# Kernel tuning notes

Hardware: AMD Instinct MI355X
Metric: run time of the kernel (lower is better)

Reference implementation:

```python
import jax, jax.numpy as jnp
import numpy as np

B, SQ, SK, D, H, HD = 2, 2048, 2048, 1024, 16, 64


def setup_inputs() -> dict:
    key = jax.random.key(0)
    ks = jax.random.split(key, 10)
    s = 1.0 / np.sqrt(D)  # keep activations well-scaled
    return {
        "x": jax.random.normal(ks[0], (B, SQ, D), jnp.float32),
        "encoder_output": jax.random.normal(ks[1], (B, SK, D), jnp.float32),
        "Wq": jax.random.normal(ks[2], (H, D, HD), jnp.float32) * s,
        "bq": jax.random.normal(ks[3], (H, HD), jnp.float32) * 0.01,
        "Wk": jax.random.normal(ks[4], (H, D, HD), jnp.float32) * s,
        "bk": jax.random.normal(ks[5], (H, HD), jnp.float32) * 0.01,
        "Wv": jax.random.normal(ks[6], (H, D, HD), jnp.float32) * s,
        "bv": jax.random.normal(ks[7], (H, HD), jnp.float32) * 0.01,
        "Wo": jax.random.normal(ks[8], (D, D), jnp.float32) * s,
        "bo": jax.random.normal(ks[9], (D,), jnp.float32) * 0.01,
    }


def reference(x, encoder_output, Wq, bq, Wk, bk, Wv, bv, Wo, bo):
    # Batched per-head projections (equivalent to the per-head nn.Linear loop).
    q = jnp.einsum('bsd,hde->bhse', x, Wq) + bq[None, :, None, :]              # [B,H,SQ,HD]
    k = jnp.einsum('bsd,hde->bhse', encoder_output, Wk) + bk[None, :, None, :]  # [B,H,SK,HD]
    v = jnp.einsum('bsd,hde->bhse', encoder_output, Wv) + bv[None, :, None, :]  # [B,H,SK,HD]
    scale = 1.0 / jnp.sqrt(jnp.asarray(HD, q.dtype))
    scores = jnp.einsum('bhqe,bhke->bhqk', q, k) * scale                        # [B,H,SQ,SK]
    attn = jax.nn.softmax(scores, axis=-1)
    out = jnp.einsum('bhqk,bhke->bhqe', attn, v)                                # [B,H,SQ,HD]
    # concat heads along feature dim (head order matches torch.cat order)
    out = out.transpose(0, 2, 1, 3).reshape(out.shape[0], out.shape[2], -1)     # [B,SQ,D]
    # final linear; dropout is identity in eval mode
    return out @ Wo + bo
```

## Files before the change

### kernel.cpp

```cpp
#include <hip/hip_runtime.h>


typedef unsigned short u16;
typedef __bf16 bf16x8 __attribute__((ext_vector_type(8)));
typedef float f32x4 __attribute__((ext_vector_type(4)));

#define B_ 2
#define SQ_ 2048
#define SK_ 2048
#define D_ 1024
#define H_ 16
#define HD_ 64

__device__ __forceinline__ u16 f2bf(float f) {
  union { float f; unsigned u; } c; c.f = f;
  unsigned u = c.u;
  return (u16)((u + 0x7fffu + ((u >> 16) & 1u)) >> 16);
}
__device__ __forceinline__ float bf2f(u16 h) {
  union { unsigned u; float f; } c; c.u = ((unsigned)h) << 16;
  return c.f;
}
__device__ __forceinline__ unsigned pack_bf16(float lo, float hi) {
  union { __bf16 h[2]; unsigned u; } c;
  c.h[0] = (__bf16)lo;
  c.h[1] = (__bf16)hi;
  return c.u;
}

#define GLOAD_LDS16(gp, lp)                                                  \
  __builtin_amdgcn_global_load_lds(                                          \
      (const __attribute__((address_space(1))) void*)(gp),                   \
      (__attribute__((address_space(3))) void*)(lp), 16, 0, 0)

__global__ __launch_bounds__(256) void cast2_f32_bf16(const float* __restrict__ x,
                                                      const float* __restrict__ enc,
                                                      u16* __restrict__ xb,
                                                      u16* __restrict__ eb) {
  const float* in = blockIdx.z ? enc : x;
  u16* out = blockIdx.z ? eb : xb;
  int i = blockIdx.x * 256 + threadIdx.x;
  float4 v = ((const float4*)in)[i];
  uint2 p;
  p.x = (unsigned)f2bf(v.x) | ((unsigned)f2bf(v.y) << 16);
  p.y = (unsigned)f2bf(v.z) | ((unsigned)f2bf(v.w) << 16);
  ((uint2*)out)[i] = p;
}

__global__ __launch_bounds__(256) void wqkv_trans(const float* __restrict__ Wq,
                                                  const float* __restrict__ Wk,
                                                  const float* __restrict__ Wv,
                                                  u16* __restrict__ out) {
  __shared__ float tile[64][65];
  const int mat = blockIdx.z >> 4, head = blockIdx.z & 15;
  const float* W = (mat == 0) ? Wq : (mat == 1 ? Wk : Wv);
  const float* ib = W + (long)head * 65536;
  u16* ob = out + ((long)mat << 20) + (long)head * 65536;
  int r0 = blockIdx.y << 6;
  int tid = threadIdx.x;
#pragma unroll
  for (int i = 0; i < 16; ++i) {
    int idx = tid + (i << 8);
    int r = idx >> 6, c = idx & 63;
    tile[r][c] = ib[(long)(r0 + r) * 64 + c];
  }
  __syncthreads();
#pragma unroll
  for (int i = 0; i < 16; ++i) {
    int idx = tid + (i << 8);
    int cc = idx >> 6, rr = idx & 63;
    ob[(long)cc * 1024 + (r0 + rr)] = f2bf(tile[rr][cc]);
  }
}

__global__ __launch_bounds__(256) void transpose_to_bf16(const float* __restrict__ in,
                                                         u16* __restrict__ out,
                                                         int R, int C,
                                                         long ibs, long obs) {
  __shared__ float tile[64][65];
  const float* ib = in + (long)blockIdx.z * ibs;
  u16* ob = out + (long)blockIdx.z * obs;
  int r0 = blockIdx.y << 6, c0 = blockIdx.x << 6;
  int tid = threadIdx.x;
#pragma unroll
  for (int i = 0; i < 16; ++i) {
    int idx = tid + (i << 8);
    int r = idx >> 6, c = idx & 63;
    tile[r][c] = ib[(long)(r0 + r) * C + (c0 + c)];
  }
  __syncthreads();
#pragma unroll
  for (int i = 0; i < 16; ++i) {
    int idx = tid + (i << 8);
    int cc = idx >> 6, rr = idx & 63;
    ob[(long)(c0 + cc) * R + (r0 + rr)] = f2bf(tile[rr][cc]);
  }
}

__global__ __launch_bounds__(256) void gemm_qkv(const u16* __restrict__ xb,
                                                const u16* __restrict__ eb,
                                                const u16* __restrict__ Wt3,
                                                const float* __restrict__ bq,
                                                const float* __restrict__ bk,
                                                const float* __restrict__ bv,
                                                u16* __restrict__ qws,
                                                u16* __restrict__ kws,
                                                u16* __restrict__ vT) {
  constexpr int M = 2048, N = 1024, K = 1024;
  __shared__ __align__(16) u16 As[128 * 32];
  __shared__ __align__(16) u16 Bs[128 * 32];
  const int tid = threadIdx.x;
  const int lane = tid & 63;
  const int wid = tid >> 6;
  const int l16 = lane & 15, quad = lane >> 4;
  const int wm = wid >> 1, wn = wid & 1;
  const int bn0g = blockIdx.x << 7;
  const int seg = bn0g >> 10;
  const int bn0 = bn0g & (N - 1);
  const int bm0 = blockIdx.y << 7;
  const u16* A = (seg == 0) ? xb : eb;
  const u16* Wt = Wt3 + ((long)seg << 20);
  const float* bias = (seg == 0) ? bq : (seg == 1 ? bk : bv);
  const long abase = (long)blockIdx.z * M * K;

  f32x4 acc[4][4];
#pragma unroll
  for (int i = 0; i < 4; ++i)
#pragma unroll
    for (int j = 0; j < 4; ++j) acc[i][j] = f32x4{0.f, 0.f, 0.f, 0.f};

  const int r0 = tid >> 2;
  const int c0s = (tid & 3) << 3;
  const u16* agp = A + abase + (long)(bm0 + r0) * K + c0s;
  const u16* bgp = Wt + (long)(bn0 + r0) * K + c0s;
  u16* alp = As + tid * 8;
  u16* blp = Bs + tid * 8;

  for (int k0 = 0; k0 < K; k0 += 32) {
    GLOAD_LDS16(agp + k0, alp);
    GLOAD_LDS16(agp + k0 + (long)64 * K, alp + 2048);
    GLOAD_LDS16(bgp + k0, blp);
    GLOAD_LDS16(bgp + k0 + (long)64 * K, blp + 2048);
    __syncthreads();
    bf16x8 af[4], bfr[4];
#pragma unroll
    for (int mi = 0; mi < 4; ++mi)
      af[mi] = *(const bf16x8*)(As + (wm * 64 + mi * 16 + l16) * 32 + quad * 8);
#pragma unroll
    for (int ni = 0; ni < 4; ++ni)
      bfr[ni] = *(const bf16x8*)(Bs + (wn * 64 + ni * 16 + l16) * 32 + quad * 8);
#pragma unroll
    for (int mi = 0; mi < 4; ++mi)
#pragma unroll
      for (int ni = 0; ni < 4; ++ni)
        acc[mi][ni] = __builtin_amdgcn_mfma_f32_16x16x32_bf16(af[mi], bfr[ni],
                                                              acc[mi][ni], 0, 0, 0);
    __syncthreads();
  }

  float bv4[4];
#pragma unroll
  for (int ni = 0; ni < 4; ++ni) bv4[ni] = bias[bn0 + wn * 64 + ni * 16 + l16];

  if (seg == 2) {
    const long zb = (long)blockIdx.z * N * M;
#pragma unroll
    for (int mi = 0; mi < 4; ++mi)
#pragma unroll
      for (int ni = 0; ni < 4; ++ni) {
        int colg = bn0 + wn * 64 + ni * 16 + l16;
        int rowg = bm0 + wm * 64 + mi * 16 + (quad << 2);
        ushort4 pk = make_ushort4(f2bf(acc[mi][ni][0] + bv4[ni]),
                                  f2bf(acc[mi][ni][1] + bv4[ni]),
                                  f2bf(acc[mi][ni][2] + bv4[ni]),
                                  f2bf(acc[mi][ni][3] + bv4[ni]));
        *(ushort4*)(vT + zb + (long)colg * M + rowg) = pk;
      }
  } else {
    u16* outp = seg ? kws : qws;
    const long cbase = (long)blockIdx.z * M * N;
#pragma unroll
    for (int mi = 0; mi < 4; ++mi)
#pragma unroll
      for (int ni = 0; ni < 4; ++ni)
#pragma unroll
        for (int r = 0; r < 4; ++r) {
          int row = bm0 + wm * 64 + mi * 16 + (quad << 2) + r;
          int col = bn0 + wn * 64 + ni * 16 + l16;
          outp[cbase + (long)row * N + col] = f2bf(acc[mi][ni][r] + bv4[ni]);
        }
  }
}

__global__ __launch_bounds__(256) void gemm_final(const u16* __restrict__ A,
                                                  const u16* __restrict__ Wt,
                                                  const float* __restrict__ bias,
                                                  float* __restrict__ C) {
  constexpr int M = 2048, N = 1024, K = 1024;
  __shared__ __align__(16) u16 As[64 * 32];
  __shared__ __align__(16) u16 Bs[128 * 32];
  const int tid = threadIdx.x;
  const int lane = tid & 63;
  const int wid = tid >> 6;
  const int l16 = lane & 15, quad = lane >> 4;
  const int bn0 = blockIdx.x << 7, bm0 = blockIdx.y << 6;

  f32x4 acc[4][2];
#pragma unroll
  for (int i = 0; i < 4; ++i)
#pragma unroll
    for (int j = 0; j < 2; ++j) acc[i][j] = f32x4{0.f, 0.f, 0.f, 0.f};

  const int r0 = tid >> 2;
  const int c0s = (tid & 3) << 3;
  const long abase = (long)blockIdx.z * M * K;
  const u16* agp = A + abase + (long)(bm0 + r0) * K + c0s;
  const u16* bgp = Wt + (long)(bn0 + r0) * K + c0s;
  u16* alp = As + tid * 8;
  u16* blp = Bs + tid * 8;

  for (int k0 = 0; k0 < K; k0 += 32) {
    GLOAD_LDS16(agp + k0, alp);
    GLOAD_LDS16(bgp + k0, blp);
    GLOAD_LDS16(bgp + k0 + (long)64 * K, blp + 2048);
    __syncthreads();
    bf16x8 af[4], bfr[2];
#pragma unroll
    for (int mi = 0; mi < 4; ++mi)
      af[mi] = *(const bf16x8*)(As + (mi * 16 + l16) * 32 + quad * 8);
#pragma unroll
    for (int ni = 0; ni < 2; ++ni)
      bfr[ni] = *(const bf16x8*)(Bs + (wid * 32 + ni * 16 + l16) * 32 + quad * 8);
#pragma unroll
    for (int mi = 0; mi < 4; ++mi)
#pragma unroll
      for (int ni = 0; ni < 2; ++ni)
        acc[mi][ni] = __builtin_amdgcn_mfma_f32_16x16x32_bf16(af[mi], bfr[ni],
                                                              acc[mi][ni], 0, 0, 0);
    __syncthreads();
  }

  float bv2[2];
#pragma unroll
  for (int ni = 0; ni < 2; ++ni) bv2[ni] = bias[bn0 + wid * 32 + ni * 16 + l16];
  const long cbase = (long)blockIdx.z * M * N;
#pragma unroll
  for (int mi = 0; mi < 4; ++mi)
#pragma unroll
    for (int ni = 0; ni < 2; ++ni)
#pragma unroll
      for (int r = 0; r < 4; ++r) {
        int row = bm0 + mi * 16 + (quad << 2) + r;
        int col = bn0 + wid * 32 + ni * 16 + l16;
        C[cbase + (long)row * N + col] = acc[mi][ni][r] + bv2[ni];
      }
}

#define ATTN_STAGE(kpp, vpp, bb)                                             \
  do {                                                                       \
    GLOAD_LDS16((kpp), Ks[bb] + tid * 8);                                    \
    GLOAD_LDS16((kpp) + (long)32 * D_, Ks[bb] + 2048 + tid * 8);             \
    GLOAD_LDS16((vpp), Vs[bb] + tid * 8);                                    \
    GLOAD_LDS16((vpp) + (long)32 * SK_, Vs[bb] + 2048 + tid * 8);            \
  } while (0)

__global__ __launch_bounds__(256, 4) void attn_flash(const u16* __restrict__ q,
                                                     const u16* __restrict__ k,
                                                     const u16* __restrict__ vT,
                                                     u16* __restrict__ ctx) {
  __shared__ __align__(16) u16 Ks[2][64 * 64];
  __shared__ __align__(16) u16 Vs[2][64 * 64];

  const int tid = threadIdx.x;
  const int lane = tid & 63;
  const int wid = tid >> 6;
  const int l16 = lane & 15, quad = lane >> 4;
  const int q0 = (blockIdx.x << 6) + (wid << 4);
  const int h = blockIdx.y, b = blockIdx.z;

  const u16* qp = q + ((long)(b * SQ_ + q0 + l16) * D_ + h * HD_ + quad * 8);
  bf16x8 a0 = *(const bf16x8*)(qp);
  bf16x8 a1 = *(const bf16x8*)(qp + 32);

  const int srow = tid >> 3, sch = tid & 7;
  const int ssw = ((sch ^ (srow & 7)) << 3);
  const u16* kp = k + ((long)(b * SK_ + srow) * D_ + h * HD_ + ssw);
  const u16* vp = vT + ((long)(b * D_ + h * HD_ + srow) * SK_ + ssw);

  const int ksw0 = ((quad ^ (l16 & 7)) << 3);
  const int ksw1 = (((quad + 4) ^ (l16 & 7)) << 3);
  const int srcA = l16 + ((quad & 1) << 5);
  const bool hisel = quad >= 2;

  float ps = 0.f;
  f32x4 o[4];
#pragma unroll
  for (int et = 0; et < 4; ++et) o[et] = f32x4{0.f, 0.f, 0.f, 0.f};

  ATTN_STAGE(kp, vp, 0);
  kp += (long)64 * D_;
  vp += 64;

  for (int c = 0; c < 32; ++c) {
    const int cur = c & 1;
    __syncthreads();
    if (c < 31) {
      ATTN_STAGE(kp, vp, cur ^ 1);
      kp += (long)64 * D_;
      vp += 64;
    }
    const u16* Kb = Ks[cur];
    const u16* Vb = Vs[cur];

    unsigned pk[4][2];
#pragma unroll
    for (int nt = 0; nt < 4; ++nt) {
      const u16* kr = Kb + (((nt << 4) + l16) << 6);
      bf16x8 kf0 = *(const bf16x8*)(kr + ksw0);
      bf16x8 kf1 = *(const bf16x8*)(kr + ksw1);
      f32x4 acc = {0.f, 0.f, 0.f, 0.f};
      acc = __builtin_amdgcn_mfma_f32_16x16x32_bf16(kf0, a0, acc, 0, 0, 0);
      acc = __builtin_amdgcn_mfma_f32_16x16x32_bf16(kf1, a1, acc, 0, 0, 0);
      float p0 = __expf(acc[0] * 0.125f);
      float p1 = __expf(acc[1] * 0.125f);
      float p2 = __expf(acc[2] * 0.125f);
      float p3 = __expf(acc[3] * 0.125f);
      ps += (p0 + p1) + (p2 + p3);
      pk[nt][0] = pack_bf16(p0, p1);
      pk[nt][1] = pack_bf16(p2, p3);
    }

#pragma unroll
    for (int kt = 0; kt < 2; ++kt) {
      int uA0 = __shfl((int)pk[2 * kt][0], srcA, 64);
      int uA1 = __shfl((int)pk[2 * kt + 1][0], srcA, 64);
      int vA0 = __shfl((int)pk[2 * kt][1], srcA, 64);
      int vA1 = __shfl((int)pk[2 * kt + 1][1], srcA, 64);
      int uB0 = __shfl((int)pk[2 * kt][0], srcA + 16, 64);
      int uB1 = __shfl((int)pk[2 * kt + 1][0], srcA + 16, 64);
      int vB0 = __shfl((int)pk[2 * kt][1], srcA + 16, 64);
      int vB1 = __shfl((int)pk[2 * kt + 1][1], srcA + 16, 64);
      union { int u[4]; bf16x8 v; } pa;
      pa.u[0] = hisel ? uA1 : uA0;
      pa.u[1] = hisel ? vA1 : vA0;
      pa.u[2] = hisel ? uB1 : uB0;
      pa.u[3] = hisel ? vB1 : vB0;
#pragma unroll
      for (int et = 0; et < 4; ++et) {
        const int e = (et << 4) + l16;
        bf16x8 bvf = *(const bf16x8*)(Vb + (e << 6) +
                                      ((((kt << 2) + quad) ^ (l16 & 7)) << 3));
        o[et] = __builtin_amdgcn_mfma_f32_16x16x32_bf16(pa.v, bvf, o[et], 0, 0, 0);
      }
    }
  }

  ps += __shfl_xor(ps, 16, 64);
  ps += __shfl_xor(ps, 32, 64);
  float inv = 1.f / ps;
  float dq[4];
#pragma unroll
  for (int r = 0; r < 4; ++r) dq[r] = __shfl(inv, (quad << 2) + r, 64);

#pragma unroll
  for (int et = 0; et < 4; ++et)
#pragma unroll
    for (int r = 0; r < 4; ++r) {
      int row = (quad << 2) + r;
      ctx[(long)(b * SQ_ + q0 + row) * D_ + h * HD_ + et * 16 + l16] =
          f2bf(o[et][r] * dq[r]);
    }
}

extern "C" void kernel_launch(void* const* d_in, const int* in_sizes, int n_in,
                              void* d_out, int out_size, void* d_ws, size_t ws_size,
                              hipStream_t stream) {
  const float* x   = (const float*)d_in[0];
  const float* enc = (const float*)d_in[1];
  const float* Wq  = (const float*)d_in[2];
  const float* bq  = (const float*)d_in[3];
  const float* Wk  = (const float*)d_in[4];
  const float* bk  = (const float*)d_in[5];
  const float* Wv  = (const float*)d_in[6];
  const float* bv  = (const float*)d_in[7];
  const float* Wo  = (const float*)d_in[8];
  const float* bo  = (const float*)d_in[9];

  const long NE_X = (long)B_ * SQ_ * D_;
  const long NE_W = (long)D_ * D_;

  u16* outA = (u16*)d_out;
  u16* outB = outA + NE_X;
  u16* eb  = outB;
  u16* vTp = outA;

  u16* ws  = (u16*)d_ws;
  u16* WqT = ws;
  u16* WoT = WqT + 3 * NE_W;
  u16* qws = WoT + NE_W;
  u16* kws = qws + NE_X;
  u16* xb  = kws + NE_X;
  u16* ctx = xb;

  cast2_f32_bf16<<<dim3((unsigned)(NE_X / 4 / 256), 1, 2), 256, 0, stream>>>(x, enc, xb, eb);

  wqkv_trans<<<dim3(1, 16, 48), 256, 0, stream>>>(Wq, Wk, Wv, WqT);
  transpose_to_bf16<<<dim3(16, 16, 1), 256, 0, stream>>>(Wo, WoT, 1024, 1024, 0L, 0L);

  gemm_qkv<<<dim3(24, 16, 2), 256, 0, stream>>>(xb, eb, WqT, bq, bk, bv,
                                                qws, kws, vTp);

  attn_flash<<<dim3(SQ_ / 64, H_, B_), 256, 0, stream>>>(qws, kws, vTp, ctx);

  gemm_final<<<dim3(8, 32, 2), 256, 0, stream>>>(ctx, WoT, bo, (float*)d_out);
}
```

Baseline: 248.7 us.

## Rewrite attention with 32x32x16 MFMA tiles and permlane32 swaps

The attention kernel now uses 32x32x16 bf16 MFMAs, with each wave handling 32 query rows, so each block covers 128 rows and the grid is halved. The P matrix is rearranged between lanes with permlane32_swap instead of many __shfl calls. s_setprio is raised around the MFMA sections, and launch bounds drop to 2 blocks per CU. The aim is fewer LDS reads and shuffles per unit of MFMA work, at the cost of higher register pressure and lower occupancy.

```diff
diff --git a/kernel.cpp b/kernel.cpp
--- a/kernel.cpp
+++ b/kernel.cpp
@@ -4,6 +4,8 @@
 typedef unsigned short u16;
 typedef __bf16 bf16x8 __attribute__((ext_vector_type(8)));
 typedef float f32x4 __attribute__((ext_vector_type(4)));
+typedef float f32x16 __attribute__((ext_vector_type(16)));
+typedef unsigned u32x2 __attribute__((ext_vector_type(2)));
 
 #define B_ 2
 #define SQ_ 2048
@@ -256,48 +258,65 @@
       }
 }
 
-#define ATTN_STAGE(kpp, vpp, bb)                                             \
-  do {                                                                       \
-    GLOAD_LDS16((kpp), Ks[bb] + tid * 8);                                    \
-    GLOAD_LDS16((kpp) + (long)32 * D_, Ks[bb] + 2048 + tid * 8);             \
-    GLOAD_LDS16((vpp), Vs[bb] + tid * 8);                                    \
-    GLOAD_LDS16((vpp) + (long)32 * SK_, Vs[bb] + 2048 + tid * 8);            \
+#define ATTN_STAGE(bb)                                                        \
+  do {                                                                        \
+    GLOAD_LDS16(kp, Ks + ((bb) << 12) + tid * 8);                             \
+    GLOAD_LDS16(kp + (long)32 * D_, Ks + ((bb) << 12) + 2048 + tid * 8);      \
+    GLOAD_LDS16(vp, Vs + ((bb) << 12) + tid * 8);                             \
+    GLOAD_LDS16(vp + (long)32 * SK_, Vs + ((bb) << 12) + 2048 + tid * 8);     \
   } while (0)
 
-__global__ __launch_bounds__(256, 4) void attn_flash(const u16* __restrict__ q,
+#define PV_KS(dd, k1, ks)                                                     \
+  do {                                                                        \
+    u32x2 sA = __builtin_amdgcn_permlane32_swap(dd[4 * (k1)],                 \
+                                                dd[4 * (k1) + 2], false,      \
+                                                false);                       \
+    u32x2 sB = __builtin_amdgcn_permlane32_swap(dd[4 * (k1) + 1],             \
+                                                dd[4 * (k1) + 3], false,      \
+                                                false);                       \
+    union { unsigned u[4]; bf16x8 v; } pa;                                    \
+    pa.u[0] = sA[0]; pa.u[1] = sB[0]; pa.u[2] = sA[1]; pa.u[3] = sB[1];       \
+    bf16x8 v0 = *(const bf16x8*)(Vb + ro0 + sw[ks]);                          \
+    bf16x8 v1 = *(const bf16x8*)(Vb + 2048 + ro0 + sw[ks]);                   \
+    o0 = __builtin_amdgcn_mfma_f32_32x32x16_bf16(pa.v, v0, o0, 0, 0, 0);      \
+    o1 = __builtin_amdgcn_mfma_f32_32x32x16_bf16(pa.v, v1, o1, 0, 0, 0);      \
+  } while (0)
+
+__global__ __launch_bounds__(256, 2) void attn_flash(const u16* __restrict__ q,
                                                      const u16* __restrict__ k,
                                                      const u16* __restrict__ vT,
                                                      u16* __restrict__ ctx) {
-  __shared__ __align__(16) u16 Ks[2][64 * 64];
-  __shared__ __align__(16) u16 Vs[2][64 * 64];
+  __shared__ __align__(16) u16 Ks[2 * 4096];
+  __shared__ __align__(16) u16 Vs[2 * 4096];
 
   const int tid = threadIdx.x;
   const int lane = tid & 63;
   const int wid = tid >> 6;
-  const int l16 = lane & 15, quad = lane >> 4;
-  const int q0 = (blockIdx.x << 6) + (wid << 4);
+  const int l31 = lane & 31, h5 = lane >> 5;
   const int h = blockIdx.y, b = blockIdx.z;
-
-  const u16* qp = q + ((long)(b * SQ_ + q0 + l16) * D_ + h * HD_ + quad * 8);
-  bf16x8 a0 = *(const bf16x8*)(qp);
-  bf16x8 a1 = *(const bf16x8*)(qp + 32);
-
-  const int srow = tid >> 3, sch = tid & 7;
-  const int ssw = ((sch ^ (srow & 7)) << 3);
+  const int q0w = (blockIdx.x << 7) + (wid << 5);
+
+  bf16x8 qf[4];
+  const u16* qp = q + ((long)(b * SQ_ + q0w + l31) * D_ + h * HD_ + 8 * h5);
+#pragma unroll
+  for (int j = 0; j < 4; ++j) qf[j] = *(const bf16x8*)(qp + 16 * j);
+
+  const int srow = tid >> 3;
+  const int ssw = ((tid & 7) ^ (srow & 7)) << 3;
   const u16* kp = k + ((long)(b * SK_ + srow) * D_ + h * HD_ + ssw);
   const u16* vp = vT + ((long)(b * D_ + h * HD_ + srow) * SK_ + ssw);
 
-  const int ksw0 = ((quad ^ (l16 & 7)) << 3);
-  const int ksw1 = (((quad + 4) ^ (l16 & 7)) << 3);
-  const int srcA = l16 + ((quad & 1) << 5);
-  const bool hisel = quad >= 2;
-
-  float ps = 0.f;
-  f32x4 o[4];
-#pragma unroll
-  for (int et = 0; et < 4; ++et) o[et] = f32x4{0.f, 0.f, 0.f, 0.f};
-
-  ATTN_STAGE(kp, vp, 0);
+  const int ro0 = l31 << 6;
+  int sw[4];
+#pragma unroll
+  for (int i = 0; i < 4; ++i) sw[i] = ((2 * i + h5) ^ (lane & 7)) << 3;
+
+  f32x16 o0, o1;
+#pragma unroll
+  for (int i = 0; i < 16; ++i) { o0[i] = 0.f; o1[i] = 0.f; }
+  float psA = 0.f, psB = 0.f;
+
+  ATTN_STAGE(0);
   kp += (long)64 * D_;
   vp += 64;
 
@@ -305,71 +324,59 @@
     const int cur = c & 1;
     __syncthreads();
     if (c < 31) {
-      ATTN_STAGE(kp, vp, cur ^ 1);
+      ATTN_STAGE(cur ^ 1);
       kp += (long)64 * D_;
       vp += 64;
     }
-    const u16* Kb = Ks[cur];
-    const u16* Vb = Vs[cur];
-
-    unsigned pk[4][2];
-#pragma unroll
-    for (int nt = 0; nt < 4; ++nt) {
-      const u16* kr = Kb + (((nt << 4) + l16) << 6);
-      bf16x8 kf0 = *(const bf16x8*)(kr + ksw0);
-      bf16x8 kf1 = *(const bf16x8*)(kr + ksw1);
-      f32x4 acc = {0.f, 0.f, 0.f, 0.f};
-      acc = __builtin_amdgcn_mfma_f32_16x16x32_bf16(kf0, a0, acc, 0, 0, 0);
-      acc = __builtin_amdgcn_mfma_f32_16x16x32_bf16(kf1, a1, acc, 0, 0, 0);
-      float p0 = __expf(acc[0] * 0.125f);
-      float p1 = __expf(acc[1] * 0.125f);
-      float p2 = __expf(acc[2] * 0.125f);
-      float p3 = __expf(acc[3] * 0.125f);
-      ps += (p0 + p1) + (p2 + p3);
-      pk[nt][0] = pack_bf16(p0, p1);
-      pk[nt][1] = pack_bf16(p2, p3);
+    const u16* Kb = Ks + (cur << 12);
+    const u16* Vb = Vs + (cur << 12);
+
+    f32x16 s0, s1;
+#pragma unroll
+    for (int i = 0; i < 16; ++i) { s0[i] = 0.f; s1[i] = 0.f; }
+    __builtin_amdgcn_s_setprio(1);
+#pragma unroll
+    for (int j = 0; j < 4; ++j) {
+      bf16x8 kf0 = *(const bf16x8*)(Kb + ro0 + sw[j]);
+      bf16x8 kf1 = *(const bf16x8*)(Kb + 2048 + ro0 + sw[j]);
+      s0 = __builtin_amdgcn_mfma_f32_32x32x16_bf16(kf0, qf[j], s0, 0, 0, 0);
+      s1 = __builtin_amdgcn_mfma_f32_32x32x16_bf16(kf1, qf[j], s1, 0, 0, 0);
     }
-
-#pragma unroll
-    for (int kt = 0; kt < 2; ++kt) {
-      int uA0 = __shfl((int)pk[2 * kt][0], srcA, 64);
-      int uA1 = __shfl((int)pk[2 * kt + 1][0], srcA, 64);
-      int vA0 = __shfl((int)pk[2 * kt][1], srcA, 64);
-      int vA1 = __shfl((int)pk[2 * kt + 1][1], srcA, 64);
-      int uB0 = __shfl((int)pk[2 * kt][0], srcA + 16, 64);
-      int uB1 = __shfl((int)pk[2 * kt + 1][0], srcA + 16, 64);
-      int vB0 = __shfl((int)pk[2 * kt][1], srcA + 16, 64);
-      int vB1 = __shfl((int)pk[2 * kt + 1][1], srcA + 16, 64);
-      union { int u[4]; bf16x8 v; } pa;
-      pa.u[0] = hisel ? uA1 : uA0;
-      pa.u[1] = hisel ? vA1 : vA0;
-      pa.u[2] = hisel ? uB1 : uB0;
-      pa.u[3] = hisel ? vB1 : vB0;
-#pragma unroll
-      for (int et = 0; et < 4; ++et) {
-        const int e = (et << 4) + l16;
-        bf16x8 bvf = *(const bf16x8*)(Vb + (e << 6) +
-                                      ((((kt << 2) + quad) ^ (l16 & 7)) << 3));
-        o[et] = __builtin_amdgcn_mfma_f32_16x16x32_bf16(pa.v, bvf, o[et], 0, 0, 0);
-      }
+    __builtin_amdgcn_s_setprio(0);
+
+    unsigned d0[8], d1[8];
+#pragma unroll
+    for (int g = 0; g < 8; ++g) {
+      float a0 = __expf(s0[2 * g] * 0.125f);
+      float a1 = __expf(s0[2 * g + 1] * 0.125f);
+      float b0 = __expf(s1[2 * g] * 0.125f);
+      float b1 = __expf(s1[2 * g + 1] * 0.125f);
+      psA += a0 + a1;
+      psB += b0 + b1;
+      d0[g] = pack_bf16(a0, a1);
+      d1[g] = pack_bf16(b0, b1);
     }
-  }
-
-  ps += __shfl_xor(ps, 16, 64);
+
+    __builtin_amdgcn_s_setprio(1);
+    PV_KS(d0, 0, 0);
+    PV_KS(d0, 1, 1);
+    PV_KS(d1, 0, 2);
+    PV_KS(d1, 1, 3);
+    __builtin_amdgcn_s_setprio(0);
+  }
+
+  float ps = psA + psB;
   ps += __shfl_xor(ps, 32, 64);
   float inv = 1.f / ps;
-  float dq[4];
-#pragma unroll
-  for (int r = 0; r < 4; ++r) dq[r] = __shfl(inv, (quad << 2) + r, 64);
-
-#pragma unroll
-  for (int et = 0; et < 4; ++et)
-#pragma unroll
-    for (int r = 0; r < 4; ++r) {
-      int row = (quad << 2) + r;
-      ctx[(long)(b * SQ_ + q0 + row) * D_ + h * HD_ + et * 16 + l16] =
-          f2bf(o[et][r] * dq[r]);
-    }
+
+#pragma unroll
+  for (int r = 0; r < 16; ++r) {
+    const int crow = (r & 3) + 8 * (r >> 2) + 4 * h5;
+    float dq = __shfl(inv, crow, 64);
+    long base = (long)(b * SQ_ + q0w + crow) * D_ + h * HD_ + l31;
+    ctx[base] = f2bf(o0[r] * dq);
+    ctx[base + 32] = f2bf(o1[r] * dq);
+  }
 }
 
 extern "C" void kernel_launch(void* const* d_in, const int* in_sizes, int n_in,
@@ -410,7 +417,7 @@
   gemm_qkv<<<dim3(24, 16, 2), 256, 0, stream>>>(xb, eb, WqT, bq, bk, bv,
                                                 qws, kws, vTp);
 
-  attn_flash<<<dim3(SQ_ / 64, H_, B_), 256, 0, stream>>>(qws, kws, vTp, ctx);
+  attn_flash<<<dim3(SQ_ / 128, H_, B_), 256, 0, stream>>>(qws, kws, vTp, ctx);
 
   gemm_final<<<dim3(8, 32, 2), 256, 0, stream>>>(ctx, WoT, bo, (float*)d_out);
 }
```

Result: faster. 235.6 us (-5.3%).
